# Optimization experiments

Measured on AMD Instinct MI355X. Metric: run time of the kernel, lower is better.

Reference implementation:

```python
import jax, jax.numpy as jnp
import numpy as np

N, M, NNZ, N_C, D = 4096, 4096, 262144, 4, 128
ADD_RATIO, TEMP = 0.1, 0.5


def setup_inputs() -> dict:
    key = jax.random.key(0)
    ks = jax.random.split(key, 6)
    X = jax.random.normal(ks[0], (N, D), dtype=jnp.float32)
    V = jax.random.randint(ks[1], (NNZ,), 0, N)
    E = jax.random.randint(ks[2], (NNZ,), 0, M)
    # incidence matrix consistent with the (V, E) pairs
    H = jnp.zeros((N, M), jnp.float32).at[V, E].set(1.0)
    incident_mask_prob = jax.random.uniform(ks[3], (N, M), jnp.float32, 1e-4, 1.0 - 1e-4)
    cos_weight = jax.random.normal(ks[4], (N_C, D), dtype=jnp.float32)
    eps = jax.random.uniform(ks[5], (N, M), jnp.float32, 1e-6, 1.0 - 1e-6)
    return {"X": X, "H": H, "V": V, "E": E,
            "incident_mask_prob": incident_mask_prob,
            "cos_weight": cos_weight, "eps": eps}


def _l2norm(x):
    # F.normalize(p=2, dim=-1): x / max(||x||, 1e-12)
    return x / jnp.maximum(jnp.linalg.norm(x, axis=-1, keepdims=True), 1e-12)


def reference(X, H, V, E, incident_mask_prob, cos_weight, eps):
    # scatter-mean of node embeddings into edge embeddings: eX [M, D]
    counts = jax.ops.segment_sum(jnp.ones((NNZ,), X.dtype), E, num_segments=M)
    eX = jax.ops.segment_sum(X[V], E, num_segments=M) / jnp.maximum(counts, 1.0)[:, None]

    node_fc = _l2norm(X[:, None, :] * cos_weight[None])   # [N, C, D]
    edge_fc = _l2norm(eX[:, None, :] * cos_weight[None])  # [M, C, D]
    # mean over C of per-channel cosine sims -> S [N, M]
    S = jnp.einsum('ncd,mcd->nm', node_fc, edge_fc) / N_C
    S = S.at[V, E].set(-1e30)  # mask existing incidences

    num_add = max(1, int(ADD_RATIO * NNZ))
    _, idx = jax.lax.top_k(S.reshape(-1), num_add)
    row = idx // M
    col = idx % M
    delta_H = jnp.zeros_like(H).at[row, col].set(1.0)
    enriched_H = H + delta_H

    # gumbel-sigmoid with straight-through estimator
    logit = (jnp.log(eps) - jnp.log(1.0 - eps)
             + jnp.log(incident_mask_prob + 1e-8)
             - jnp.log(1.0 - incident_mask_prob + 1e-8))
    soft = jax.nn.sigmoid(logit / TEMP)
    hard = (soft > 0.5).astype(soft.dtype)
    incident_mask = hard - jax.lax.stop_gradient(soft) + soft
    return enriched_H * incident_mask
```

## Files before the change

kernel.cpp:

```cpp
#include <hip/hip_runtime.h>

#define N_NODES 4096
#define M_EDGES 4096
#define NNZ_K   262144
#define NCH     4
#define DIM     128
#define KDIM    512
#define NM      (N_NODES * M_EDGES)
#define NUM_ADD 26214
#define NCB     2048
#define NFB     32768
#define CAP     262144
#define CAP2    65536

#define EXD_OFF   0ull
#define AFC_OFF   4194304ull
#define BFC_OFF   8388608ull
#define BKT_OFF   12582912ull
#define CVAL_OFF  13631488ull
#define CIDX_OFF  15728640ull
#define CIDX2_OFF 16777216ull
#define CNT_OFF   17039360ull
#define OFFS_OFF  17055744ull
#define CUR_OFF   17072132ull
#define HIST_OFF  17088516ull
#define FHIST_OFF 17096708ull
#define SCL_OFF   17227780ull
#define ZERO_BYTES (17227844ull - CNT_OFF)

typedef short bf16x8 __attribute__((ext_vector_type(8)));
typedef float f32x4  __attribute__((ext_vector_type(4)));

__device__ __forceinline__ int bin_c(float s) {
    int b = (int)floorf((s + 1.0f) * 1024.0f);
    return min(max(b, 0), NCB - 1);
}

__device__ __forceinline__ int fbin_of(double v, int bstar) {
    double lo = (double)(bstar - 12) * (2.0 / 2048.0) - 1.0;
    double wd = (28.0 * (2.0 / 2048.0)) / (double)NFB;
    int f = (int)floor((v - lo) / wd);
    return min(max(f, 0), NFB - 1);
}

__device__ __forceinline__ float hard_mask(float p, float e) {
    float logit = logf(e) - logf(1.0f - e) + logf(p + 1e-8f) - logf(1.0f - p + 1e-8f);
    float soft  = 1.0f / (1.0f + expf(-2.0f * logit));
    return (soft > 0.5f) ? 1.0f : 0.0f;
}

__device__ __forceinline__ unsigned short to_bf16_rtne(float f) {
    unsigned int b = __float_as_uint(f);
    b += 0x7FFFu + ((b >> 16) & 1u);
    return (unsigned short)(b >> 16);
}

__global__ void k_count(const int* __restrict__ E, int* __restrict__ cnt) {
    int k = blockIdx.x * 256 + threadIdx.x;
    if (k < NNZ_K) atomicAdd(&cnt[E[k]], 1);
}

__global__ __launch_bounds__(256) void k_scan(const int* __restrict__ cnt, int* __restrict__ offs) {
    __shared__ int part[256];
    int t = threadIdx.x;
    int loc[16]; int s = 0;
    for (int j = 0; j < 16; ++j) { loc[j] = cnt[t * 16 + j]; s += loc[j]; }
    part[t] = s;
    __syncthreads();
    if (t == 0) { int acc = 0; for (int i = 0; i < 256; ++i) { int v = part[i]; part[i] = acc; acc += v; } }
    __syncthreads();
    int acc = part[t];
    for (int j = 0; j < 16; ++j) { offs[t * 16 + j] = acc; acc += loc[j]; }
    if (t == 255) offs[4096] = acc;
}

__global__ void k_fill(const int* __restrict__ E, const int* __restrict__ offs,
                       int* __restrict__ cur, int* __restrict__ bkt) {
    int k = blockIdx.x * 256 + threadIdx.x;
    if (k < NNZ_K) {
        int e = E[k];
        int pos = atomicAdd(&cur[e], 1);
        bkt[offs[e] + pos] = k;
    }
}

__global__ __launch_bounds__(128) void k_edge_mean(
        const int* __restrict__ Vv, const int* __restrict__ cnt,
        const int* __restrict__ offs, const int* __restrict__ bkt,
        const float* __restrict__ X, double* __restrict__ eXd) {
    __shared__ int sk[1024];
    __shared__ int sv[1024];
    int m = blockIdx.x;
    int c = cnt[m]; if (c > 1024) c = 1024;
    int off = offs[m];
    for (int t = threadIdx.x; t < c; t += 128) sk[t] = bkt[off + t];
    __syncthreads();
    for (int t = threadIdx.x; t < c; t += 128) {
        int key = sk[t]; int r = 0;
        for (int j = 0; j < c; ++j) r += (sk[j] < key);
        sv[r] = Vv[key];
    }
    __syncthreads();
    int d = threadIdx.x;
    double s = 0.0;
    for (int j = 0; j < c; ++j) s += (double)X[sv[j] * DIM + d];
    eXd[m * DIM + d] = s / (double)(c > 1 ? c : 1);
}

template <typename T>
__global__ __launch_bounds__(128) void k_fc(const T* __restrict__ in,
                                            const float* __restrict__ w,
                                            unsigned short* __restrict__ out) {
    __shared__ double red[128];
    int n = blockIdx.x, d = threadIdx.x;
    double x = (double)in[n * DIM + d];
    for (int c = 0; c < NCH; ++c) {
        double v = x * (double)w[c * DIM + d];
        red[d] = v * v;
        __syncthreads();
        for (int s = 64; s > 0; s >>= 1) { if (d < s) red[d] += red[d + s]; __syncthreads(); }
        double denom = fmax(sqrt(red[0]), 1e-12);
        __syncthreads();
        out[n * KDIM + c * DIM + d] = to_bf16_rtne((float)(v / denom));
    }
}

__global__ __launch_bounds__(256) void k_gemm_mfma(const unsigned short* __restrict__ A,
                                                   const unsigned short* __restrict__ B,
                                                   float* __restrict__ S) {
    __shared__ short As[128][40];
    __shared__ short Bs[128][40];
    int tid = threadIdx.x;
    int row0 = blockIdx.y * 128, col0 = blockIdx.x * 128;
    int w = tid >> 6, l = tid & 63;
    int wr = (w >> 1) * 64, wc = (w & 1) * 64;
    f32x4 acc[4][4] = {};
    const unsigned short* src = (tid < 128) ? (A + (size_t)(row0 + tid) * KDIM)
                                            : (B + (size_t)(col0 + (tid - 128)) * KDIM);
    short* dst = (tid < 128) ? &As[tid][0] : &Bs[tid - 128][0];
    for (int k0 = 0; k0 < KDIM; k0 += 32) {
        uint4 d0 = *(const uint4*)(src + k0);
        uint4 d1 = *(const uint4*)(src + k0 + 8);
        uint4 d2 = *(const uint4*)(src + k0 + 16);
        uint4 d3 = *(const uint4*)(src + k0 + 24);
        __syncthreads();
        *(uint4*)(dst + 0)  = d0;
        *(uint4*)(dst + 8)  = d1;
        *(uint4*)(dst + 16) = d2;
        *(uint4*)(dst + 24) = d3;
        __syncthreads();
        int kq = (l >> 4) * 8;
        bf16x8 af[4], bfr[4];
        #pragma unroll
        for (int m = 0; m < 4; ++m) af[m] = *(const bf16x8*)&As[wr + m * 16 + (l & 15)][kq];
        #pragma unroll
        for (int n = 0; n < 4; ++n) bfr[n] = *(const bf16x8*)&Bs[wc + n * 16 + (l & 15)][kq];
        #pragma unroll
        for (int m = 0; m < 4; ++m)
            #pragma unroll
            for (int n = 0; n < 4; ++n)
                acc[m][n] = __builtin_amdgcn_mfma_f32_16x16x32_bf16(af[m], bfr[n], acc[m][n], 0, 0, 0);
    }
    #pragma unroll
    for (int m = 0; m < 4; ++m) {
        int r = row0 + wr + m * 16 + (l >> 4) * 4;
        #pragma unroll
        for (int n = 0; n < 4; ++n) {
            int c = col0 + wc + n * 16 + (l & 15);
            #pragma unroll
            for (int j = 0; j < 4; ++j)
                S[(size_t)(r + j) * M_EDGES + c] = 0.25f * acc[m][n][j];
        }
    }
}

__global__ void k_mask(const int* __restrict__ Vv, const int* __restrict__ E,
                       float* __restrict__ S) {
    int k = blockIdx.x * 256 + threadIdx.x;
    if (k < NNZ_K) S[(size_t)Vv[k] * M_EDGES + E[k]] = -1e30f;
}

__global__ __launch_bounds__(256) void k_hist_coarse(const float4* __restrict__ S4,
                                                     int* __restrict__ hist) {
    __shared__ int h[NCB];
    for (int i = threadIdx.x; i < NCB; i += 256) h[i] = 0;
    __syncthreads();
    int stride = gridDim.x * 256;
    for (int i = blockIdx.x * 256 + threadIdx.x; i < NM / 4; i += stride) {
        float4 v = S4[i];
        if (v.x > -2.0f) atomicAdd(&h[bin_c(v.x)], 1);
        if (v.y > -2.0f) atomicAdd(&h[bin_c(v.y)], 1);
        if (v.z > -2.0f) atomicAdd(&h[bin_c(v.z)], 1);
        if (v.w > -2.0f) atomicAdd(&h[bin_c(v.w)], 1);
    }
    __syncthreads();
    for (int i = threadIdx.x; i < NCB; i += 256)
        if (h[i]) atomicAdd(&hist[i], h[i]);
}

__global__ __launch_bounds__(256) void k_findcut(const int* __restrict__ hist, int* __restrict__ scl) {
    __shared__ int part[256];
    __shared__ int sb;
    int t = threadIdx.x;
    int loc[8]; int s = 0;
    for (int j = 0; j < 8; ++j) { loc[j] = hist[t * 8 + j]; s += loc[j]; }
    part[t] = s;
    __syncthreads();
    if (t == 0) { int acc = 0; for (int i = 255; i >= 0; --i) { int v = part[i]; part[i] = acc; acc += v; } }
    __syncthreads();
    int run = part[t];
    for (int j = 7; j >= 0; --j) {
        int h = loc[j];
        run += h;
        if (run >= NUM_ADD && run - h < NUM_ADD) { scl[0] = t * 8 + j; sb = t * 8 + j; }
    }
    __syncthreads();
    int bstar = sb;
    int g = 0;
    for (int i = bstar + 11 + t; i < NCB; i += 256) g += hist[i];
    part[t] = g;
    __syncthreads();
    for (int st2 = 128; st2 > 0; st2 >>= 1) { if (t < st2) part[t] += part[t + st2]; __syncthreads(); }
    if (t == 0) scl[1] = part[0];
}

#define LB1 4096
#define LB2 2048
__global__ __launch_bounds__(256) void k_collect(const float4* __restrict__ S4,
        int* __restrict__ scl, int* __restrict__ cidx, int* __restrict__ cidx2) {
    __shared__ int buf1[LB1];
    __shared__ int buf2[LB2];
    __shared__ int c1, c2, g1, g2;
    int t = threadIdx.x;
    if (t == 0) { c1 = 0; c2 = 0; }
    __syncthreads();
    int bstar = scl[0];
    const int total4 = NM / 4;
    for (int i0 = blockIdx.x * 256; i0 < total4; i0 += gridDim.x * 256) {
        if (c1 > LB1 - 1024 || c2 > LB2 - 1024) {
            if (t == 0) { g1 = atomicAdd(&scl[2], c1); g2 = atomicAdd(&scl[3], c2); }
            __syncthreads();
            for (int j = t; j < c1; j += 256) { int g = g1 + j; if (g < CAP)  cidx[g]  = buf1[j]; }
            for (int j = t; j < c2; j += 256) { int g = g2 + j; if (g < CAP2) cidx2[g] = buf2[j]; }
            __syncthreads();
            if (t == 0) { c1 = 0; c2 = 0; }
            __syncthreads();
        }
        int i = i0 + t;
        if (i < total4) {
            float4 v = S4[i];
            float sc;
            #define COLLECT1(comp, cc)                                         \
                sc = comp;                                                     \
                if (sc > -2.0f) {                                              \
                    int b = bin_c(sc);                                         \
                    if (b >= bstar + 11) {                                     \
                        int s2 = atomicAdd(&c2, 1);                            \
                        buf2[s2] = i * 4 + cc;                                 \
                    } else if (b >= bstar - 11) {                              \
                        int s1 = atomicAdd(&c1, 1);                            \
                        buf1[s1] = i * 4 + cc;                                 \
                    }                                                          \
                }
            COLLECT1(v.x, 0) COLLECT1(v.y, 1) COLLECT1(v.z, 2) COLLECT1(v.w, 3)
            #undef COLLECT1
        }
        __syncthreads();
    }
    if (t == 0) { g1 = atomicAdd(&scl[2], c1); g2 = atomicAdd(&scl[3], c2); }
    __syncthreads();
    for (int j = t; j < c1; j += 256) { int g = g1 + j; if (g < CAP)  cidx[g]  = buf1[j]; }
    for (int j = t; j < c2; j += 256) { int g = g2 + j; if (g < CAP2) cidx2[g] = buf2[j]; }
}

__global__ void k_scatter(const int* __restrict__ Vv, const int* __restrict__ E,
                          const float* __restrict__ prob, const float* __restrict__ eps,
                          float* __restrict__ out) {
    int k = blockIdx.x * 256 + threadIdx.x;
    if (k < NNZ_K) {
        size_t idx = (size_t)Vv[k] * M_EDGES + E[k];
        out[idx] = hard_mask(prob[idx], eps[idx]);
    }
}

__global__ __launch_bounds__(256) void k_selc(const int* __restrict__ scl,
        const int* __restrict__ cidx2,
        const float* __restrict__ prob, const float* __restrict__ eps,
        float* __restrict__ out) {
    int n = scl[3]; if (n > CAP2) n = CAP2;
    for (int i = blockIdx.x * 256 + threadIdx.x; i < n; i += 256 * 128) {
        int idx = cidx2[i];
        out[idx] = hard_mask(prob[idx], eps[idx]);
    }
}

__global__ __launch_bounds__(256) void k_exact(
        const int* __restrict__ scl, const int* __restrict__ cidx, double* __restrict__ cval,
        const float* __restrict__ X, const double* __restrict__ eXd, const float* __restrict__ cw) {
    int nc = scl[2]; if (nc > CAP) nc = CAP;
    for (int i = blockIdx.x * 256 + threadIdx.x; i < nc; i += 256 * 512) {
        int idx = cidx[i];
        int n = idx >> 12, m = idx & (M_EDGES - 1);
        double acc = 0.0;
        for (int c = 0; c < NCH; ++c) {
            double dn = 0.0, de = 0.0, dt = 0.0;
            for (int d = 0; d < DIM; ++d) {
                double w  = (double)cw[c * DIM + d];
                double xn = (double)X[n * DIM + d] * w;
                double xe = eXd[m * DIM + d] * w;
                dn += xn * xn; de += xe * xe; dt += xn * xe;
            }
            acc += dt / (fmax(sqrt(dn), 1e-12) * fmax(sqrt(de), 1e-12));
        }
        cval[i] = acc * 0.25;
    }
}

__global__ __launch_bounds__(256) void k_fhist(const int* __restrict__ scl,
                                               const int* __restrict__ cidx,
                                               const double* __restrict__ cval,
                                               int* __restrict__ fh) {
    int nc = scl[2]; if (nc > CAP) nc = CAP;
    int bstar = scl[0];
    for (int i = blockIdx.x * 256 + threadIdx.x; i < nc; i += 256 * 256)
        atomicAdd(&fh[fbin_of(cval[i], bstar)], 1);
}

__global__ __launch_bounds__(1024) void k_ffind(const int* __restrict__ fh, int* __restrict__ scl) {
    __shared__ int part[1024];
    int T = NUM_ADD - scl[1];
    int t = threadIdx.x;
    int loc[32]; int s = 0;
    for (int j = 0; j < 32; ++j) { loc[j] = fh[t * 32 + j]; s += loc[j]; }
    part[t] = s;
    __syncthreads();
    if (t == 0) { int acc = 0; for (int i = 1023; i >= 0; --i) { int v = part[i]; part[i] = acc; acc += v; } }
    __syncthreads();
    int run = part[t];
    for (int j = 31; j >= 0; --j) {
        int h = loc[j];
        run += h;
        if (run >= T && run - h < T) { scl[4] = t * 32 + j; scl[5] = run - h; }
    }
}

__global__ __launch_bounds__(256) void k_write(
        const int* __restrict__ scl, const int* __restrict__ cidx, const double* __restrict__ cval,
        const float* __restrict__ prob, const float* __restrict__ eps,
        float* __restrict__ out) {
    int nc = scl[2]; if (nc > CAP) nc = CAP;
    int fs = scl[4], bstar = scl[0];
    for (int i = blockIdx.x * 256 + threadIdx.x; i < nc; i += 256 * 256) {
        if (fbin_of(cval[i], bstar) > fs) {
            int idx = cidx[i];
            out[idx] = hard_mask(prob[idx], eps[idx]);
        }
    }
}

__global__ __launch_bounds__(256) void k_tie(
        const int* __restrict__ scl, const int* __restrict__ cidx, const double* __restrict__ cval,
        const float* __restrict__ prob, const float* __restrict__ eps,
        float* __restrict__ out) {
    __shared__ double mv[256];
    __shared__ int    mi[256];
    __shared__ int    cnt;
    int nc = scl[2]; if (nc > CAP) nc = CAP;
    int T = NUM_ADD - scl[1];
    int fs = scl[4], G1f = scl[5], bstar = scl[0];
    int t = threadIdx.x;
    if (t == 0) cnt = 0;
    __syncthreads();
    for (int i = t; i < nc; i += 256) {
        if (fbin_of(cval[i], bstar) == fs) {
            int s = atomicAdd(&cnt, 1);
            if (s < 256) { mv[s] = cval[i]; mi[s] = cidx[i]; }
        }
    }
    __syncthreads();
    int nm = min(cnt, 256);
    for (int k = t; k < nm; k += 256) {
        double v = mv[k]; int idx = mi[k];
        int rank = G1f;
        for (int j = 0; j < nm; ++j)
            rank += (mv[j] > v || (mv[j] == v && mi[j] < idx)) ? 1 : 0;
        if (rank < T)
            out[idx] = hard_mask(prob[idx], eps[idx]);
    }
}

extern "C" void kernel_launch(void* const* d_in, const int* in_sizes, int n_in,
                              void* d_out, int out_size, void* d_ws, size_t ws_size,
                              hipStream_t stream) {
    const float* X    = (const float*)d_in[0];
    const int*   Vv   = (const int*)d_in[2];
    const int*   E    = (const int*)d_in[3];
    const float* prob = (const float*)d_in[4];
    const float* cw   = (const float*)d_in[5];
    const float* eps  = (const float*)d_in[6];
    float* out = (float*)d_out;
    char*  ws  = (char*)d_ws;

    double*         eXd   = (double*)(ws + EXD_OFF);
    unsigned short* Afc   = (unsigned short*)(ws + AFC_OFF);
    unsigned short* Bfc   = (unsigned short*)(ws + BFC_OFF);
    int*            bkt   = (int*)(ws + BKT_OFF);
    double*         cval  = (double*)(ws + CVAL_OFF);
    int*            cidx  = (int*)(ws + CIDX_OFF);
    int*            cidx2 = (int*)(ws + CIDX2_OFF);
    int*            cnt   = (int*)(ws + CNT_OFF);
    int*            offs  = (int*)(ws + OFFS_OFF);
    int*            cur   = (int*)(ws + CUR_OFF);
    int*            hist  = (int*)(ws + HIST_OFF);
    int*            fh    = (int*)(ws + FHIST_OFF);
    int*            scl   = (int*)(ws + SCL_OFF);

    hipMemsetAsync(ws + CNT_OFF, 0, (size_t)ZERO_BYTES, stream);

    k_count<<<NNZ_K / 256, 256, 0, stream>>>(E, cnt);
    k_scan<<<1, 256, 0, stream>>>(cnt, offs);
    k_fill<<<NNZ_K / 256, 256, 0, stream>>>(E, offs, cur, bkt);
    k_edge_mean<<<M_EDGES, 128, 0, stream>>>(Vv, cnt, offs, bkt, X, eXd);
    k_fc<float><<<N_NODES, 128, 0, stream>>>(X, cw, Afc);
    k_fc<double><<<M_EDGES, 128, 0, stream>>>(eXd, cw, Bfc);
    dim3 gg(M_EDGES / 128, N_NODES / 128);
    k_gemm_mfma<<<gg, 256, 0, stream>>>(Afc, Bfc, out);
    k_mask<<<NNZ_K / 256, 256, 0, stream>>>(Vv, E, out);
    k_hist_coarse<<<1024, 256, 0, stream>>>((const float4*)out, hist);
    k_findcut<<<1, 256, 0, stream>>>(hist, scl);
    k_collect<<<1024, 256, 0, stream>>>((const float4*)out, scl, cidx, cidx2);
    hipMemsetAsync(out, 0, (size_t)NM * sizeof(float), stream);
    k_scatter<<<NNZ_K / 256, 256, 0, stream>>>(Vv, E, prob, eps, out);
    k_selc<<<128, 256, 0, stream>>>(scl, cidx2, prob, eps, out);
    k_exact<<<512, 256, 0, stream>>>(scl, cidx, cval, X, eXd, cw);
    k_fhist<<<256, 256, 0, stream>>>(scl, cidx, cval, fh);
    k_ffind<<<1, 1024, 0, stream>>>(fh, scl);
    k_write<<<256, 256, 0, stream>>>(scl, cidx, cval, prob, eps, out);
    k_tie<<<1, 256, 0, stream>>>(scl, cidx, cval, prob, eps, out);
}
```

Measured before the change: 328.4 us.

## Use direct global-to-LDS loads in GEMM and replicate histogram bins

The GEMM tile loads now go straight from global memory into LDS through global_load_lds (16 bytes per lane), replacing the register-staged copy. The LDS row padding is dropped to match the contiguous layout that instruction writes. Separately, the coarse histogram keeps four privatized LDS copies selected by thread index, so fewer lanes contend on the same shared-memory atomics, and the copies are summed before the global atomic flush. Removing the padding may add LDS bank conflicts on the MFMA fragment reads, and the GEMM still has no double buffering.

```diff
diff --git a/kernel.cpp b/kernel.cpp
--- a/kernel.cpp
+++ b/kernel.cpp
@@ -30,6 +30,11 @@
 
 typedef short bf16x8 __attribute__((ext_vector_type(8)));
 typedef float f32x4  __attribute__((ext_vector_type(4)));
+
+#define GLOAD_LDS16(gsrc, ldst)                                                 \
+    __builtin_amdgcn_global_load_lds(                                           \
+        (const __attribute__((address_space(1))) void*)(gsrc),                  \
+        (__attribute__((address_space(3))) void*)(ldst), 16, 0, 0)
 
 __device__ __forceinline__ int bin_c(float s) {
     int b = (int)floorf((s + 1.0f) * 1024.0f);
@@ -128,26 +133,25 @@
 __global__ __launch_bounds__(256) void k_gemm_mfma(const unsigned short* __restrict__ A,
                                                    const unsigned short* __restrict__ B,
                                                    float* __restrict__ S) {
-    __shared__ short As[128][40];
-    __shared__ short Bs[128][40];
+    __shared__ short As[128][32];
+    __shared__ short Bs[128][32];
     int tid = threadIdx.x;
     int row0 = blockIdx.y * 128, col0 = blockIdx.x * 128;
     int w = tid >> 6, l = tid & 63;
     int wr = (w >> 1) * 64, wc = (w & 1) * 64;
     f32x4 acc[4][4] = {};
-    const unsigned short* src = (tid < 128) ? (A + (size_t)(row0 + tid) * KDIM)
-                                            : (B + (size_t)(col0 + (tid - 128)) * KDIM);
-    short* dst = (tid < 128) ? &As[tid][0] : &Bs[tid - 128][0];
+    int lrow = l >> 2, lcol = (l & 3) * 8;
+    int rb0 = (w * 2 + 0) * 16, rb1 = (w * 2 + 1) * 16;
+    const unsigned short* sA0 = A + (size_t)(row0 + rb0 + lrow) * KDIM + lcol;
+    const unsigned short* sA1 = A + (size_t)(row0 + rb1 + lrow) * KDIM + lcol;
+    const unsigned short* sB0 = B + (size_t)(col0 + rb0 + lrow) * KDIM + lcol;
+    const unsigned short* sB1 = B + (size_t)(col0 + rb1 + lrow) * KDIM + lcol;
     for (int k0 = 0; k0 < KDIM; k0 += 32) {
-        uint4 d0 = *(const uint4*)(src + k0);
-        uint4 d1 = *(const uint4*)(src + k0 + 8);
-        uint4 d2 = *(const uint4*)(src + k0 + 16);
-        uint4 d3 = *(const uint4*)(src + k0 + 24);
         __syncthreads();
-        *(uint4*)(dst + 0)  = d0;
-        *(uint4*)(dst + 8)  = d1;
-        *(uint4*)(dst + 16) = d2;
-        *(uint4*)(dst + 24) = d3;
+        GLOAD_LDS16(sA0 + k0, &As[rb0][0]);
+        GLOAD_LDS16(sA1 + k0, &As[rb1][0]);
+        GLOAD_LDS16(sB0 + k0, &Bs[rb0][0]);
+        GLOAD_LDS16(sB1 + k0, &Bs[rb1][0]);
         __syncthreads();
         int kq = (l >> 4) * 8;
         bf16x8 af[4], bfr[4];
@@ -182,20 +186,24 @@
 
 __global__ __launch_bounds__(256) void k_hist_coarse(const float4* __restrict__ S4,
                                                      int* __restrict__ hist) {
-    __shared__ int h[NCB];
-    for (int i = threadIdx.x; i < NCB; i += 256) h[i] = 0;
-    __syncthreads();
+    __shared__ int h[4][NCB + 8];
+    int t = threadIdx.x;
+    for (int i = t; i < 4 * (NCB + 8); i += 256) ((int*)h)[i] = 0;
+    __syncthreads();
+    int* hc = h[t & 3];
     int stride = gridDim.x * 256;
-    for (int i = blockIdx.x * 256 + threadIdx.x; i < NM / 4; i += stride) {
+    for (int i = blockIdx.x * 256 + t; i < NM / 4; i += stride) {
         float4 v = S4[i];
-        if (v.x > -2.0f) atomicAdd(&h[bin_c(v.x)], 1);
-        if (v.y > -2.0f) atomicAdd(&h[bin_c(v.y)], 1);
-        if (v.z > -2.0f) atomicAdd(&h[bin_c(v.z)], 1);
-        if (v.w > -2.0f) atomicAdd(&h[bin_c(v.w)], 1);
-    }
-    __syncthreads();
-    for (int i = threadIdx.x; i < NCB; i += 256)
-        if (h[i]) atomicAdd(&hist[i], h[i]);
+        if (v.x > -2.0f) atomicAdd(&hc[bin_c(v.x)], 1);
+        if (v.y > -2.0f) atomicAdd(&hc[bin_c(v.y)], 1);
+        if (v.z > -2.0f) atomicAdd(&hc[bin_c(v.z)], 1);
+        if (v.w > -2.0f) atomicAdd(&hc[bin_c(v.w)], 1);
+    }
+    __syncthreads();
+    for (int i = t; i < NCB; i += 256) {
+        int s = h[0][i] + h[1][i] + h[2][i] + h[3][i];
+        if (s) atomicAdd(&hist[i], s);
+    }
 }
 
 __global__ __launch_bounds__(256) void k_findcut(const int* __restrict__ hist, int* __restrict__ scl) {
```

After: 313.6 us. -4.5%, faster.
